# Kernel optimization log

Measured on AMD Instinct MI355X. Metric: run time of the kernel, lower is better.

## Reference

```python
import jax, jax.numpy as jnp
import numpy as np

B, N, F_IN, F_HID, F_OUT = 64, 1024, 64, 128, 64

def setup_inputs() -> dict:
    key = jax.random.key(0)
    ks = jax.random.split(key, 6)
    x = jax.random.normal(ks[0], (B, N, F_IN), dtype=jnp.float32)
    adj = jax.random.uniform(ks[1], (B, N, N), dtype=jnp.float32)
    mask = jax.random.randint(ks[2], (B, N), 0, 2).astype(bool)
    W1 = jax.random.normal(ks[3], (F_IN, F_HID), dtype=jnp.float32) * (1.0 / np.sqrt(F_IN))
    b1 = jnp.zeros((F_HID,), dtype=jnp.float32)
    W2 = jax.random.normal(ks[4], (F_HID, F_OUT), dtype=jnp.float32) * (1.0 / np.sqrt(F_HID))
    b2 = jnp.zeros((F_OUT,), dtype=jnp.float32)
    eps = jnp.zeros((1,), dtype=jnp.float32)
    return {"x": x, "adj": adj, "mask": mask, "W1": W1, "b1": b1, "W2": W2, "b2": b2, "eps": eps}

def reference(x, adj, mask, W1, b1, W2, b2, eps):
    # neighbor aggregation: out[b,i,f] = sum_j adj[b,i,j] * x[b,j,f]
    agg = jnp.einsum('bij,bjf->bif', adj, x)
    # add_loop=True: (1 + eps) * x + aggregated neighbors
    h = (1.0 + eps[0]) * x + agg
    # 2-layer GIN MLP applied per node (only valid nodes contribute in the
    # torch version via gather/scatter; invalid positions are zeroed)
    h = jax.nn.relu(h @ W1 + b1) @ W2 + b2
    return jnp.where(mask[..., None], h, jnp.zeros((), dtype=h.dtype))
```

## Files before the change

kernel.cpp:

```cpp
#include <hip/hip_runtime.h>


#define N_    1024
#define FIN   64
#define FHID  128
#define FOUT  64
#define HS_LD 68
#define H1_LD 132
#define FROW  9

typedef __attribute__((ext_vector_type(16))) float f32x16;
typedef __attribute__((ext_vector_type(8)))  short s16x8;

__device__ inline short f2bf(float f) {
    union { float f; unsigned int u; } v; v.f = f;
    unsigned int r = v.u + 0x7fffu + ((v.u >> 16) & 1u);
    return (short)(r >> 16);
}

__global__ __launch_bounds__(256) void gin_fused(
    const float* __restrict__ x, const float* __restrict__ adj,
    const int* __restrict__ mask, const float* __restrict__ W1,
    const float* __restrict__ b1, const float* __restrict__ W2,
    const float* __restrict__ b2, const float* __restrict__ epsp,
    float* __restrict__ out)
{
    __shared__ s16x8 region1[2112];
    __shared__ float hs[64 * HS_LD];

    s16x8 (*asf)[FROW] = reinterpret_cast<s16x8 (*)[FROW]>(region1);
    s16x8 (*xtf)[FROW] = reinterpret_cast<s16x8 (*)[FROW]>(region1 + 576);
    float* h1s = reinterpret_cast<float*>(region1);

    const int t    = threadIdx.x;
    const int lane = t & 63;
    const int w    = t >> 6;
    const int b    = blockIdx.x >> 4;
    const int i0   = (blockIdx.x & 15) * 64;

    const float* xb   = x   + (size_t)b * N_ * FIN;
    const float* adjb = adj + (size_t)b * N_ * N_ + (size_t)i0 * N_;

    const int l31  = lane & 31;
    const int half = lane >> 5;
    const int mrow = (w & 1) * 32;
    const int ncol = (w >> 1) * 32;

    const int sr = t >> 2;
    const int sc = (t & 3) * 16;
    const int sg = (t & 3) * 2;

    f32x16 acc;
    #pragma unroll
    for (int r = 0; r < 16; ++r) acc[r] = 0.f;

    for (int jc = 0; jc < N_ / 64; ++jc) {
        const int j0 = jc * 64;

        {
            const float* ar = adjb + (size_t)sr * N_ + j0 + sc;
            const float4 p0 = *reinterpret_cast<const float4*>(ar);
            const float4 p1 = *reinterpret_cast<const float4*>(ar + 4);
            const float4 p2 = *reinterpret_cast<const float4*>(ar + 8);
            const float4 p3 = *reinterpret_cast<const float4*>(ar + 12);
            s16x8 f0, f1;
            f0[0] = f2bf(p0.x); f0[1] = f2bf(p0.y); f0[2] = f2bf(p0.z); f0[3] = f2bf(p0.w);
            f0[4] = f2bf(p1.x); f0[5] = f2bf(p1.y); f0[6] = f2bf(p1.z); f0[7] = f2bf(p1.w);
            f1[0] = f2bf(p2.x); f1[1] = f2bf(p2.y); f1[2] = f2bf(p2.z); f1[3] = f2bf(p2.w);
            f1[4] = f2bf(p3.x); f1[5] = f2bf(p3.y); f1[6] = f2bf(p3.z); f1[7] = f2bf(p3.w);
            asf[sr][sg]     = f0;
            asf[sr][sg + 1] = f1;
        }
        {
            s16x8 q0, q1;
            #pragma unroll
            for (int jj = 0; jj < 8; ++jj)
                q0[jj] = f2bf(xb[(size_t)(j0 + w * 16 + jj) * FIN + lane]);
            #pragma unroll
            for (int jj = 0; jj < 8; ++jj)
                q1[jj] = f2bf(xb[(size_t)(j0 + w * 16 + 8 + jj) * FIN + lane]);
            xtf[lane][2 * w]     = q0;
            xtf[lane][2 * w + 1] = q1;
        }
        __syncthreads();

        #pragma unroll
        for (int s = 0; s < 4; ++s) {
            const s16x8 a  = asf[mrow + l31][2 * s + half];
            const s16x8 bf = xtf[ncol + l31][2 * s + half];
            acc = __builtin_amdgcn_mfma_f32_32x32x16_bf16(a, bf, acc, 0, 0, 0);
        }
        __syncthreads();
    }

    {
        const float se = 1.0f + epsp[0];
        const int col = ncol + l31;
        #pragma unroll
        for (int reg = 0; reg < 16; ++reg) {
            const int row = mrow + (reg & 3) + 8 * (reg >> 2) + 4 * half;
            const float xv = xb[(size_t)(i0 + row) * FIN + col];
            hs[row * HS_LD + col] = acc[reg] + se * xv;
        }
    }
    __syncthreads();

    {
        const int k4 = (t & 31) * 4;
        const int rb = (t >> 5) * 8;
        float4 hacc[8];
        const float4 b1v = *reinterpret_cast<const float4*>(b1 + k4);
        #pragma unroll
        for (int r = 0; r < 8; ++r) hacc[r] = b1v;

        #pragma unroll 4
        for (int j = 0; j < FIN; ++j) {
            const float4 w1v = *reinterpret_cast<const float4*>(W1 + j * FHID + k4);
            #pragma unroll
            for (int r = 0; r < 8; ++r) {
                const float hv = hs[(rb + r) * HS_LD + j];
                hacc[r].x += hv * w1v.x; hacc[r].y += hv * w1v.y;
                hacc[r].z += hv * w1v.z; hacc[r].w += hv * w1v.w;
            }
        }
        #pragma unroll
        for (int r = 0; r < 8; ++r) {
            float4 v;
            v.x = fmaxf(hacc[r].x, 0.f); v.y = fmaxf(hacc[r].y, 0.f);
            v.z = fmaxf(hacc[r].z, 0.f); v.w = fmaxf(hacc[r].w, 0.f);
            *reinterpret_cast<float4*>(&h1s[(rb + r) * H1_LD + k4]) = v;
        }
    }
    __syncthreads();

    {
        const int fi = (t & 15) * 4;
        const int ri = (t >> 4) * 4;
        float4 oacc[4];
        const float4 b2v = *reinterpret_cast<const float4*>(b2 + fi);
        #pragma unroll
        for (int ii = 0; ii < 4; ++ii) oacc[ii] = b2v;

        #pragma unroll 4
        for (int j = 0; j < FHID; ++j) {
            const float4 w2v = *reinterpret_cast<const float4*>(W2 + j * FOUT + fi);
            #pragma unroll
            for (int ii = 0; ii < 4; ++ii) {
                const float hv = h1s[(ri + ii) * H1_LD + j];
                oacc[ii].x += hv * w2v.x; oacc[ii].y += hv * w2v.y;
                oacc[ii].z += hv * w2v.z; oacc[ii].w += hv * w2v.w;
            }
        }
        #pragma unroll
        for (int ii = 0; ii < 4; ++ii) {
            const int gi = i0 + ri + ii;
            const int m  = mask[b * N_ + gi];
            float4 o = oacc[ii];
            if (!m) o = make_float4(0.f, 0.f, 0.f, 0.f);
            *reinterpret_cast<float4*>(out + ((size_t)b * N_ + gi) * FOUT + fi) = o;
        }
    }
}

extern "C" void kernel_launch(void* const* d_in, const int* in_sizes, int n_in,
                              void* d_out, int out_size, void* d_ws, size_t ws_size,
                              hipStream_t stream) {
    const float* x    = (const float*)d_in[0];
    const float* adj  = (const float*)d_in[1];
    const int*   mask = (const int*)  d_in[2];
    const float* W1   = (const float*)d_in[3];
    const float* b1   = (const float*)d_in[4];
    const float* W2   = (const float*)d_in[5];
    const float* b2   = (const float*)d_in[6];
    const float* eps  = (const float*)d_in[7];
    float* out = (float*)d_out;

    dim3 grid(64 * 16);
    dim3 block(256);
    gin_fused<<<grid, block, 0, stream>>>(x, adj, mask, W1, b1, W2, b2, eps, out);
}
```

Baseline: 428.4 us.

## Prepack x to bf16 fragments and double-buffer adjacency tiles with register prefetch

Adds a separate pre-pass kernel that converts x into bf16 MFMA B-fragment layout in workspace, so the main kernel loads B operands straight into registers instead of staging transposed x through shared memory. The adjacency K-chunk grows from 64 to 128 columns and uses a double-buffered LDS tile with register prefetch of the next chunk, which cuts the number of barriers and overlaps global loads with MFMAs. The cost is an extra kernel launch and a workspace round trip for x, more registers (occupancy hint of 3 blocks per CU), and a larger LDS footprint.

New measurement: 416.0 us. 2.9% less time.

```diff
diff --git a/kernel.cpp b/kernel.cpp
--- a/kernel.cpp
+++ b/kernel.cpp
@@ -1,13 +1,15 @@
 #include <hip/hip_runtime.h>
 
 
-#define N_    1024
-#define FIN   64
-#define FHID  128
-#define FOUT  64
-#define HS_LD 68
-#define H1_LD 132
-#define FROW  9
+#define N_     1024
+#define FIN    64
+#define FHID   128
+#define FOUT   64
+#define HS_LD  68
+#define H1_LD  132
+#define FROW   17
+#define NCHUNK 8
+#define KSPC   8
 
 typedef __attribute__((ext_vector_type(16))) float f32x16;
 typedef __attribute__((ext_vector_type(8)))  short s16x8;
@@ -18,19 +20,39 @@
     return (short)(r >> 16);
 }
 
-__global__ __launch_bounds__(256) void gin_fused(
+__global__ __launch_bounds__(256) void xt_pack(const float* __restrict__ x,
+                                               s16x8* __restrict__ xt)
+{
+    const int g  = blockIdx.x * 256 + threadIdx.x;
+    const int n  = g & 31;
+    const int ng = (g >> 5) & 1;
+    const int ks = (g >> 6) & 63;
+    const int b  = g >> 12;
+    const int f  = ng * 32 + n;
+
+    s16x8 u0, u1;
+    #pragma unroll
+    for (int k = 0; k < 8; ++k)
+        u0[k] = f2bf(x[(size_t)(b * N_ + ks * 16 + k) * FIN + f]);
+    #pragma unroll
+    for (int k = 0; k < 8; ++k)
+        u1[k] = f2bf(x[(size_t)(b * N_ + ks * 16 + 8 + k) * FIN + f]);
+    xt[2 * g]     = u0;
+    xt[2 * g + 1] = u1;
+}
+
+__global__ __launch_bounds__(256, 3) void gin_main(
     const float* __restrict__ x, const float* __restrict__ adj,
     const int* __restrict__ mask, const float* __restrict__ W1,
     const float* __restrict__ b1, const float* __restrict__ W2,
     const float* __restrict__ b2, const float* __restrict__ epsp,
-    float* __restrict__ out)
+    const s16x8* __restrict__ xt, float* __restrict__ out)
 {
-    __shared__ s16x8 region1[2112];
+    __shared__ s16x8 region[2 * 64 * FROW];
     __shared__ float hs[64 * HS_LD];
 
-    s16x8 (*asf)[FROW] = reinterpret_cast<s16x8 (*)[FROW]>(region1);
-    s16x8 (*xtf)[FROW] = reinterpret_cast<s16x8 (*)[FROW]>(region1 + 576);
-    float* h1s = reinterpret_cast<float*>(region1);
+    s16x8 (*asf)[64][FROW] = reinterpret_cast<s16x8 (*)[64][FROW]>(region);
+    float* h1s = reinterpret_cast<float*>(region);
 
     const int t    = threadIdx.x;
     const int lane = t & 63;
@@ -45,52 +67,68 @@
     const int half = lane >> 5;
     const int mrow = (w & 1) * 32;
     const int ncol = (w >> 1) * 32;
-
-    const int sr = t >> 2;
-    const int sc = (t & 3) * 16;
-    const int sg = (t & 3) * 2;
+    const int ngq  = (w >> 1);
+
+    const int sr  = t >> 2;
+    const int scf = (t & 3) * 32;
+    const int sfg = (t & 3) * 4;
+    const float* arow_p = adjb + (size_t)sr * N_ + scf;
+
+    const int bfl = l31 * 2 + half;
+    const size_t bgbase = (size_t)(b * 64) * 2 + ngq;
 
     f32x16 acc;
     #pragma unroll
     for (int r = 0; r < 16; ++r) acc[r] = 0.f;
 
-    for (int jc = 0; jc < N_ / 64; ++jc) {
-        const int j0 = jc * 64;
-
-        {
-            const float* ar = adjb + (size_t)sr * N_ + j0 + sc;
-            const float4 p0 = *reinterpret_cast<const float4*>(ar);
-            const float4 p1 = *reinterpret_cast<const float4*>(ar + 4);
-            const float4 p2 = *reinterpret_cast<const float4*>(ar + 8);
-            const float4 p3 = *reinterpret_cast<const float4*>(ar + 12);
-            s16x8 f0, f1;
-            f0[0] = f2bf(p0.x); f0[1] = f2bf(p0.y); f0[2] = f2bf(p0.z); f0[3] = f2bf(p0.w);
-            f0[4] = f2bf(p1.x); f0[5] = f2bf(p1.y); f0[6] = f2bf(p1.z); f0[7] = f2bf(p1.w);
-            f1[0] = f2bf(p2.x); f1[1] = f2bf(p2.y); f1[2] = f2bf(p2.z); f1[3] = f2bf(p2.w);
-            f1[4] = f2bf(p3.x); f1[5] = f2bf(p3.y); f1[6] = f2bf(p3.z); f1[7] = f2bf(p3.w);
-            asf[sr][sg]     = f0;
-            asf[sr][sg + 1] = f1;
-        }
-        {
-            s16x8 q0, q1;
-            #pragma unroll
-            for (int jj = 0; jj < 8; ++jj)
-                q0[jj] = f2bf(xb[(size_t)(j0 + w * 16 + jj) * FIN + lane]);
-            #pragma unroll
-            for (int jj = 0; jj < 8; ++jj)
-                q1[jj] = f2bf(xb[(size_t)(j0 + w * 16 + 8 + jj) * FIN + lane]);
-            xtf[lane][2 * w]     = q0;
-            xtf[lane][2 * w + 1] = q1;
-        }
-        __syncthreads();
-
-        #pragma unroll
-        for (int s = 0; s < 4; ++s) {
-            const s16x8 a  = asf[mrow + l31][2 * s + half];
-            const s16x8 bf = xtf[ncol + l31][2 * s + half];
-            acc = __builtin_amdgcn_mfma_f32_32x32x16_bf16(a, bf, acc, 0, 0, 0);
-        }
-        __syncthreads();
+    float4 pa[8];
+    s16x8  pbc[KSPC];
+    s16x8  pbn[KSPC];
+
+    #pragma unroll
+    for (int q = 0; q < 8; ++q)
+        pa[q] = *reinterpret_cast<const float4*>(arow_p + 0 * 128 + q * 4);
+    #pragma unroll
+    for (int s = 0; s < KSPC; ++s)
+        pbc[s] = xt[(bgbase + (size_t)(0 * KSPC + s) * 2) * 64 + bfl];
+    #pragma unroll
+    for (int q = 0; q < 4; ++q) {
+        const float4 u = pa[2 * q], v = pa[2 * q + 1];
+        s16x8 fr;
+        fr[0] = f2bf(u.x); fr[1] = f2bf(u.y); fr[2] = f2bf(u.z); fr[3] = f2bf(u.w);
+        fr[4] = f2bf(v.x); fr[5] = f2bf(v.y); fr[6] = f2bf(v.z); fr[7] = f2bf(v.w);
+        asf[0][sr][sfg + q] = fr;
+    }
+    __syncthreads();
+
+    #pragma unroll
+    for (int c = 0; c < NCHUNK; ++c) {
+        if (c + 1 < NCHUNK) {
+            #pragma unroll
+            for (int q = 0; q < 8; ++q)
+                pa[q] = *reinterpret_cast<const float4*>(arow_p + (c + 1) * 128 + q * 4);
+            #pragma unroll
+            for (int s = 0; s < KSPC; ++s)
+                pbn[s] = xt[(bgbase + (size_t)((c + 1) * KSPC + s) * 2) * 64 + bfl];
+        }
+        #pragma unroll
+        for (int s = 0; s < KSPC; ++s) {
+            const s16x8 a = asf[c & 1][mrow + l31][2 * s + half];
+            acc = __builtin_amdgcn_mfma_f32_32x32x16_bf16(a, pbc[s], acc, 0, 0, 0);
+        }
+        if (c + 1 < NCHUNK) {
+            #pragma unroll
+            for (int q = 0; q < 4; ++q) {
+                const float4 u = pa[2 * q], v = pa[2 * q + 1];
+                s16x8 fr;
+                fr[0] = f2bf(u.x); fr[1] = f2bf(u.y); fr[2] = f2bf(u.z); fr[3] = f2bf(u.w);
+                fr[4] = f2bf(v.x); fr[5] = f2bf(v.y); fr[6] = f2bf(v.z); fr[7] = f2bf(v.w);
+                asf[(c + 1) & 1][sr][sfg + q] = fr;
+            }
+            #pragma unroll
+            for (int s = 0; s < KSPC; ++s) pbc[s] = pbn[s];
+            __syncthreads();
+        }
     }
 
     {
@@ -174,8 +212,8 @@
     const float* b2   = (const float*)d_in[6];
     const float* eps  = (const float*)d_in[7];
     float* out = (float*)d_out;
-
-    dim3 grid(64 * 16);
-    dim3 block(256);
-    gin_fused<<<grid, block, 0, stream>>>(x, adj, mask, W1, b1, W2, b2, eps, out);
-}
+    s16x8* xt = (s16x8*)d_ws;
+
+    xt_pack<<<dim3(1024), dim3(256), 0, stream>>>(x, xt);
+    gin_main<<<dim3(64 * 16), dim3(256), 0, stream>>>(x, adj, mask, W1, b1, W2, b2, eps, xt, out);
+}
```
